# Kernel optimization log

Measured on AMD Instinct MI355X. Metric: run time of the kernel, lower is better.

## Reference

```python
import jax, jax.numpy as jnp
import numpy as np

NUM_HEADS = 8
NEG_INF = -2**32 + 1  # matches the TF code's masking constant


def setup_inputs() -> dict:
    key = jax.random.key(0)
    ks = jax.random.split(key, 12)
    B, L, D_IN, D_MODEL = 2, 2048, 256, 256
    s = 1.0 / np.sqrt(D_IN)
    return {
        "queries": jax.random.normal(ks[0], (B, L, D_IN), jnp.float32),
        "keys": jax.random.normal(ks[1], (B, L, D_IN), jnp.float32),
        "values": jax.random.normal(ks[2], (B, L, D_IN), jnp.float32),
        "key_mask": jax.random.randint(ks[3], (B, L, 1), 0, 2, jnp.int32),
        "Wq": jax.random.normal(ks[4], (D_IN, D_MODEL), jnp.float32) * s,
        "bq": jnp.zeros((D_MODEL,), jnp.float32),
        "Wk": jax.random.normal(ks[5], (D_IN, D_MODEL), jnp.float32) * s,
        "bk": jnp.zeros((D_MODEL,), jnp.float32),
        "Wv": jax.random.normal(ks[6], (D_IN, D_MODEL), jnp.float32) * s,
        "bv": jnp.zeros((D_MODEL,), jnp.float32),
        "Wo": jax.random.normal(ks[7], (D_MODEL, D_IN), jnp.float32) * s,
        "bo": jnp.zeros((D_IN,), jnp.float32),
    }


def reference(queries, keys, values, key_mask, Wq, bq, Wk, bk, Wv, bv, Wo, bo):
    B, Lq, _ = queries.shape
    Lk = keys.shape[1]
    h = NUM_HEADS
    d_model = Wq.shape[1]
    depth = d_model // h

    Q = queries @ Wq + bq  # [B, Lq, d_model]
    K = keys @ Wk + bk     # [B, Lk, d_model]
    V = values @ Wv + bv   # [B, Lk, d_model]

    # split heads: contiguous chunks of size depth along feature dim
    Qh = Q.reshape(B, Lq, h, depth)
    Kh = K.reshape(B, Lk, h, depth)
    Vh = V.reshape(B, Lk, h, depth)

    scores = jnp.einsum("bqhd,bkhd->bhqk", Qh, Kh) / jnp.sqrt(
        jnp.asarray(depth, jnp.float32)
    )  # [B, h, Lq, Lk]

    # key_mask: [B, Lk, 1] -> broadcast over heads and query positions
    mask = (key_mask[:, None, :, 0] != 0)[:, :, None, :]  # [B, 1, 1, Lk]
    scores = jnp.where(mask, scores, jnp.asarray(NEG_INF, scores.dtype))

    attn = jax.nn.softmax(scores, axis=-1)  # dropout is identity at inference
    out = jnp.einsum("bhqk,bkhd->bqhd", attn, Vh).reshape(B, Lq, d_model)
    return out @ Wo + bo  # [B, Lq, input_dim]
```

## Files before the change

kernel.cpp:

```cpp
#include <hip/hip_runtime.h>

#define Bn 2
#define Ln 2048
#define DIN 256
#define Hn 8
#define DEPTH 32
#define SCALE 0.17677669529663687f
#define NEGC (-4294967296.0f)
#define NG  (Ln / 16)
#define WLS 264

typedef _Float16 f16;
typedef _Float16 h8 __attribute__((ext_vector_type(8)));
typedef _Float16 h4 __attribute__((ext_vector_type(4)));
typedef float f4 __attribute__((ext_vector_type(4)));


__global__ __launch_bounds__(256) void proj_gemm(
    const float* __restrict__ Xq, const float* __restrict__ Xk, const float* __restrict__ Xv,
    const float* __restrict__ Wq, const float* __restrict__ Wk, const float* __restrict__ Wv,
    const float* __restrict__ bq, const float* __restrict__ bk, const float* __restrict__ bv,
    f16* __restrict__ Qz, f16* __restrict__ Kz, f16* __restrict__ Vz)
{
    const int p = blockIdx.z;
    const float* X = p == 0 ? Xq : p == 1 ? Xk : Xv;
    const float* W = p == 0 ? Wq : p == 1 ? Wk : Wv;
    const float* bias = p == 0 ? bq : p == 1 ? bk : bv;

    const int t = threadIdx.x, w = t >> 6, lane = t & 63;
    const int l15 = lane & 15, quad = lane >> 4;
    const int n0 = blockIdx.y * 64;
    const int m0 = blockIdx.x * 64 + w * 16;

    const float* A0 = X + (size_t)(m0 + l15) * DIN;
    const float* Wp = W + n0 + l15;

    f4 acc[4] = {{0.f,0.f,0.f,0.f},{0.f,0.f,0.f,0.f},
                 {0.f,0.f,0.f,0.f},{0.f,0.f,0.f,0.f}};
    #pragma unroll
    for (int kk = 0; kk < 8; ++kk) {
        const int k0 = kk * 32;
        float4 xa = *(const float4*)(A0 + k0 + quad * 8);
        float4 xb = *(const float4*)(A0 + k0 + quad * 8 + 4);
        h8 af = { (f16)xa.x, (f16)xa.y, (f16)xa.z, (f16)xa.w,
                  (f16)xb.x, (f16)xb.y, (f16)xb.z, (f16)xb.w };
        h8 bf[4];
        #pragma unroll
        for (int tt = 0; tt < 4; ++tt)
            #pragma unroll
            for (int j = 0; j < 8; ++j)
                bf[tt][j] = (f16)Wp[(size_t)(k0 + quad * 8 + j) * DIN + tt * 16];
        #pragma unroll
        for (int tt = 0; tt < 4; ++tt)
            acc[tt] = __builtin_amdgcn_mfma_f32_16x16x32_f16(af, bf[tt], acc[tt], 0, 0, 0);
    }
    #pragma unroll
    for (int tt = 0; tt < 4; ++tt) {
        const int c = n0 + tt * 16 + l15;
        const float bb = bias[c];
        const int h = c >> 5, dd = c & 31;
        #pragma unroll
        for (int r = 0; r < 4; ++r) {
            const int row = m0 + quad * 4 + r;
            const int b = row >> 11, l = row & (Ln - 1);
            const float v = acc[tt][r] + bb;
            const size_t hbg = (size_t)(b * Hn + h) * NG + (l >> 4);
            if (p == 0)
                Qz[(hbg * 64 + (dd >> 3) * 16 + (l & 15)) * 8 + (dd & 7)] =
                    (f16)(v * SCALE);
            else if (p == 1)
                Kz[(hbg * 64 + (dd >> 3) * 16 + (l & 15)) * 8 + (dd & 7)] = (f16)v;
            else
                Vz[((hbg * 2 + (dd >> 4)) * 64 + ((l & 15) >> 2) * 16 + (dd & 15)) * 4
                   + (l & 3)] = (f16)v;
        }
    }
}

__global__ __launch_bounds__(512) void flash_mfma(
    const f16* __restrict__ Qz, const f16* __restrict__ Kz,
    const f16* __restrict__ Vz, const int* __restrict__ mask,
    f16* __restrict__ Oz)
{
    __shared__ float Os[8][32][34];
    __shared__ float lS[8][32];
    const int t = threadIdx.x, w = t >> 6, lane = t & 63;
    const int l15 = lane & 15, quad = lane >> 4;
    const int bid = blockIdx.x;
    const int swz = (bid & 7) * 128 + (bid >> 3);
    const int hb = swz >> 6, qc = swz & 63;
    const int q0 = qc * 32;
    const int b = hb >> 3, h = hb & 7;
    const f16* Qh = Qz + (size_t)hb * NG * 512;
    const f16* Kh = Kz + (size_t)hb * NG * 512;
    const f16* Vh = Vz + (size_t)hb * NG * 512;
    const int* mrow = mask + b * Ln;
    const int k_base = w * (Ln / 8);

    h8 qf[2];
    #pragma unroll
    for (int qg = 0; qg < 2; ++qg)
        qf[qg] = *(const h8*)(Qh + ((size_t)(qc * 2 + qg) * 64 + lane) * 8);

    f4 o[2][2];
    #pragma unroll
    for (int i = 0; i < 2; ++i)
        #pragma unroll
        for (int j = 0; j < 2; ++j) o[i][j] = (f4){0.f, 0.f, 0.f, 0.f};
    float l_run[2] = {0.f, 0.f};

    for (int kt = 0; kt < Ln / 8 / 64; ++kt) {
        const int k0 = k_base + kt * 64;
        #pragma unroll
        for (int tt = 0; tt < 4; ++tt) {
            const int g = (k0 >> 4) + tt;
            h8 kf = *(const h8*)(Kh + ((size_t)g * 64 + lane) * 8);
            const int4 mk = *(const int4*)(mrow + g * 16 + quad * 4);
            f4 bias4 = { mk.x ? 0.f : NEGC, mk.y ? 0.f : NEGC,
                         mk.z ? 0.f : NEGC, mk.w ? 0.f : NEGC };
            h4 va0 = *(const h4*)(Vh + ((size_t)(g * 2)     * 64 + lane) * 4);
            h4 va1 = *(const h4*)(Vh + ((size_t)(g * 2 + 1) * 64 + lane) * 4);
            f4 s[2];
            #pragma unroll
            for (int qg = 0; qg < 2; ++qg)
                s[qg] = __builtin_amdgcn_mfma_f32_16x16x32_f16(kf, qf[qg], bias4, 0, 0, 0);
            #pragma unroll
            for (int qg = 0; qg < 2; ++qg) {
                h4 pf;
                #pragma unroll
                for (int r = 0; r < 4; ++r) {
                    const float pv = __expf(s[qg][r]);
                    l_run[qg] += pv;
                    pf[r] = (f16)pv;
                }
                o[0][qg] = __builtin_amdgcn_mfma_f32_16x16x16f16(va0, pf, o[0][qg], 0, 0, 0);
                o[1][qg] = __builtin_amdgcn_mfma_f32_16x16x16f16(va1, pf, o[1][qg], 0, 0, 0);
            }
        }
    }
    #pragma unroll
    for (int qg = 0; qg < 2; ++qg) {
        l_run[qg] += __shfl_xor(l_run[qg], 16, 64);
        l_run[qg] += __shfl_xor(l_run[qg], 32, 64);
        if (quad == 0) lS[w][qg * 16 + l15] = l_run[qg];
        #pragma unroll
        for (int dg = 0; dg < 2; ++dg)
            #pragma unroll
            for (int r = 0; r < 4; ++r)
                Os[w][dg * 16 + quad * 4 + r][qg * 16 + l15] = o[dg][qg][r];
    }
    __syncthreads();

    if (t < 128) {
        const int cq = t & 31, dv = t >> 5;
        float ls = 0.f;
        #pragma unroll
        for (int i = 0; i < 8; ++i) ls += lS[i][cq];
        const float inv = 1.0f / ls;
        h8 pack;
        #pragma unroll
        for (int i = 0; i < 8; ++i) {
            const int dd = dv * 8 + i;
            float ov = 0.f;
            #pragma unroll
            for (int s = 0; s < 8; ++s) ov += Os[s][dd][cq];
            pack[i] = (f16)(ov * inv);
        }
        const int gm = b * NG + ((q0 + cq) >> 4);
        *(h8*)(Oz + (((size_t)gm * 8 + h) * 64 + dv * 16 + (cq & 15)) * 8) = pack;
    }
}

__global__ __launch_bounds__(256) void out_gemm(
    const f16* __restrict__ Oz, const float* __restrict__ Wo,
    const float* __restrict__ bo, float* __restrict__ out)
{
    const int t = threadIdx.x, w = t >> 6, lane = t & 63;
    const int l15 = lane & 15, quad = lane >> 4;
    const int g = blockIdx.x >> 1, nh = blockIdx.x & 1;

    h8 af[8];
    #pragma unroll
    for (int h = 0; h < 8; ++h)
        af[h] = *(const h8*)(Oz + (((size_t)g * 8 + h) * 64 + lane) * 8);

    const float* Wop = Wo + nh * 128 + w * 32 + l15;
    f4 acc[2] = {{0.f,0.f,0.f,0.f},{0.f,0.f,0.f,0.f}};
    #pragma unroll
    for (int h = 0; h < 8; ++h) {
        h8 bf[2];
        #pragma unroll
        for (int tt = 0; tt < 2; ++tt)
            #pragma unroll
            for (int j = 0; j < 8; ++j)
                bf[tt][j] = (f16)Wop[(size_t)(h * 32 + quad * 8 + j) * DIN + tt * 16];
        #pragma unroll
        for (int tt = 0; tt < 2; ++tt)
            acc[tt] = __builtin_amdgcn_mfma_f32_16x16x32_f16(af[h], bf[tt], acc[tt], 0, 0, 0);
    }
    #pragma unroll
    for (int tt = 0; tt < 2; ++tt) {
        const int c = nh * 128 + w * 32 + tt * 16 + l15;
        const float bb = bo[c];
        #pragma unroll
        for (int r = 0; r < 4; ++r)
            out[(size_t)(g * 16 + quad * 4 + r) * DIN + c] = acc[tt][r] + bb;
    }
}

__global__ __launch_bounds__(256) void fb_projKV(
    const float* __restrict__ Xk, const float* __restrict__ Xv,
    const float* __restrict__ Wk, const float* __restrict__ Wv,
    const float* __restrict__ bk, const float* __restrict__ bv,
    f16* S, int b)
{
    __shared__ f16 Wl[64 * WLS];
    const int p = blockIdx.z;
    const float* X = (p ? Xv : Xk) + (size_t)b * Ln * DIN;
    const float* W = p ? Wv : Wk;
    const float* bias = p ? bv : bk;

    const int t = threadIdx.x, w = t >> 6, lane = t & 63;
    const int l15 = lane & 15, quad = lane >> 4;
    const int n0 = blockIdx.y * 64;

    {
        const int nl = t & 63, kb = t >> 6;
        for (int kk = 0; kk < 64; ++kk) {
            const int k = kk * 4 + kb;
            Wl[nl * WLS + k] = (f16)W[(size_t)k * DIN + n0 + nl];
        }
    }
    __syncthreads();

    const int m0w = blockIdx.x * 128 + w * 32;
    const float* A0 = X + (size_t)(m0w + l15) * DIN;
    const float* A1 = X + (size_t)(m0w + 16 + l15) * DIN;

    f4 acc[2][4];
    #pragma unroll
    for (int mi = 0; mi < 2; ++mi)
        #pragma unroll
        for (int tt = 0; tt < 4; ++tt) acc[mi][tt] = (f4){0.f, 0.f, 0.f, 0.f};

    for (int k0 = 0; k0 < DIN; k0 += 32) {
        float4 xa0 = *(const float4*)(A0 + k0 + quad * 8);
        float4 xb0 = *(const float4*)(A0 + k0 + quad * 8 + 4);
        float4 xa1 = *(const float4*)(A1 + k0 + quad * 8);
        float4 xb1 = *(const float4*)(A1 + k0 + quad * 8 + 4);
        h8 af0 = { (f16)xa0.x, (f16)xa0.y, (f16)xa0.z, (f16)xa0.w,
                   (f16)xb0.x, (f16)xb0.y, (f16)xb0.z, (f16)xb0.w };
        h8 af1 = { (f16)xa1.x, (f16)xa1.y, (f16)xa1.z, (f16)xa1.w,
                   (f16)xb1.x, (f16)xb1.y, (f16)xb1.z, (f16)xb1.w };
        #pragma unroll
        for (int tt = 0; tt < 4; ++tt) {
            h8 bf = *(const h8*)(Wl + (tt * 16 + l15) * WLS + k0 + quad * 8);
            acc[0][tt] = __builtin_amdgcn_mfma_f32_16x16x32_f16(af0, bf, acc[0][tt], 0, 0, 0);
            acc[1][tt] = __builtin_amdgcn_mfma_f32_16x16x32_f16(af1, bf, acc[1][tt], 0, 0, 0);
        }
    }
    #pragma unroll
    for (int mi = 0; mi < 2; ++mi)
        #pragma unroll
        for (int tt = 0; tt < 4; ++tt) {
            const int c = n0 + tt * 16 + l15;
            const float bb = bias[c];
            const int h = c >> 5, dd = c & 31;
            #pragma unroll
            for (int r = 0; r < 4; ++r) {
                const int l = m0w + mi * 16 + quad * 4 + r;
                const float v = acc[mi][tt][r] + bb;
                const unsigned hg = (unsigned)h * 128 + (l >> 4);
                unsigned j;
                if (!p)
                    j = (hg * 64 + (unsigned)(dd >> 3) * 16 + (l & 15)) * 8 + (dd & 7);
                else
                    j = 524288u + ((hg * 2 + (dd >> 4)) * 64
                        + (unsigned)((l & 15) >> 2) * 16 + (dd & 15)) * 4 + (l & 3);
                S[(((size_t)(j >> 12)) << 13) + 4096u + (j & 4095u)] = (f16)v;
            }
        }
}

__global__ __launch_bounds__(512) void fb_flashQ(
    const float* __restrict__ Xq, const float* __restrict__ Wq,
    const float* __restrict__ bq, const int* __restrict__ mask,
    float* outbuf, int b)
{
    __shared__ union {
        struct { f16 Wlq[32 * WLS]; f16 Qs[2048]; } a;
        struct { float Os[8][32][68]; float lS[8][64]; } c;
    } sm;
    f16* S = (f16*)outbuf;
    const int t = threadIdx.x, w = t >> 6, lane = t & 63;
    const int l15 = lane & 15, quad = lane >> 4;
    const int h = blockIdx.x, q0 = blockIdx.y * 64;

    {
        const int nl = t & 31, kb = t >> 5;
        for (int kk = 0; kk < 16; ++kk) {
            const int k = kk * 16 + kb;
            sm.a.Wlq[nl * WLS + k] = (f16)Wq[(size_t)k * DIN + h * 32 + nl];
        }
    }
    __syncthreads();

    if (w < 4) {
        const float* A0 = Xq + (size_t)(b * Ln + q0 + w * 16 + l15) * DIN;
        f4 a2[2] = { {0.f,0.f,0.f,0.f}, {0.f,0.f,0.f,0.f} };
        #pragma unroll
        for (int kk = 0; kk < 8; ++kk) {
            const int k0 = kk * 32;
            float4 xa = *(const float4*)(A0 + k0 + quad * 8);
            float4 xb = *(const float4*)(A0 + k0 + quad * 8 + 4);
            h8 af = { (f16)xa.x, (f16)xa.y, (f16)xa.z, (f16)xa.w,
                      (f16)xb.x, (f16)xb.y, (f16)xb.z, (f16)xb.w };
            #pragma unroll
            for (int tt = 0; tt < 2; ++tt) {
                h8 bf = *(const h8*)(sm.a.Wlq + (tt * 16 + l15) * WLS + k0 + quad * 8);
                a2[tt] = __builtin_amdgcn_mfma_f32_16x16x32_f16(af, bf, a2[tt], 0, 0, 0);
            }
        }
        #pragma unroll
        for (int tt = 0; tt < 2; ++tt) {
            const int c = tt * 16 + l15;
            const float bb = bq[h * 32 + c];
            #pragma unroll
            for (int r = 0; r < 4; ++r) {
                const int lc = quad * 4 + r;
                sm.a.Qs[((size_t)w * 64 + (c >> 3) * 16 + lc) * 8 + (c & 7)] =
                    (f16)((a2[tt][r] + bb) * SCALE);
            }
        }
    }
    __syncthreads();
    h8 qf[4];
    #pragma unroll
    for (int qg = 0; qg < 4; ++qg)
        qf[qg] = *(const h8*)(sm.a.Qs + ((size_t)qg * 64 + lane) * 8);
    __syncthreads();

    const int* mrow = mask + b * Ln;
    f4 o[2][4];
    #pragma unroll
    for (int i = 0; i < 2; ++i)
        #pragma unroll
        for (int j = 0; j < 4; ++j) o[i][j] = (f4){0.f, 0.f, 0.f, 0.f};
    float l_run[4] = {0.f, 0.f, 0.f, 0.f};
    const int k_base = w * (Ln / 8);

    for (int kt = 0; kt < Ln / 8 / 64; ++kt) {
        const int k0 = k_base + kt * 64;
        #pragma unroll
        for (int tt = 0; tt < 4; ++tt) {
            const int g = (k0 >> 4) + tt;
            const size_t kaddr = ((size_t)(h * 16 + (g >> 3)) << 13) + 4096u
                               + (size_t)((g & 7) * 512 + lane * 8);
            h8 kf = *(const h8*)(S + kaddr);
            const int4 mk = *(const int4*)(mrow + g * 16 + quad * 4);
            f4 bias4 = { mk.x ? 0.f : NEGC, mk.y ? 0.f : NEGC,
                         mk.z ? 0.f : NEGC, mk.w ? 0.f : NEGC };
            const size_t vaddr = ((size_t)(128 + h * 16 + (g >> 3)) << 13) + 4096u
                               + (size_t)((g & 7) * 512 + lane * 4);
            h4 va0 = *(const h4*)(S + vaddr);
            h4 va1 = *(const h4*)(S + vaddr + 256);
            f4 s_[4];
            #pragma unroll
            for (int qg = 0; qg < 4; ++qg)
                s_[qg] = __builtin_amdgcn_mfma_f32_16x16x32_f16(kf, qf[qg], bias4, 0, 0, 0);
            #pragma unroll
            for (int qg = 0; qg < 4; ++qg) {
                h4 pf;
                #pragma unroll
                for (int r = 0; r < 4; ++r) {
                    const float pv = __expf(s_[qg][r]);
                    l_run[qg] += pv;
                    pf[r] = (f16)pv;
                }
                o[0][qg] = __builtin_amdgcn_mfma_f32_16x16x16f16(va0, pf, o[0][qg], 0, 0, 0);
                o[1][qg] = __builtin_amdgcn_mfma_f32_16x16x16f16(va1, pf, o[1][qg], 0, 0, 0);
            }
        }
    }
    #pragma unroll
    for (int qg = 0; qg < 4; ++qg) {
        l_run[qg] += __shfl_xor(l_run[qg], 16, 64);
        l_run[qg] += __shfl_xor(l_run[qg], 32, 64);
        if (quad == 0) sm.c.lS[w][qg * 16 + l15] = l_run[qg];
        #pragma unroll
        for (int dg = 0; dg < 2; ++dg)
            #pragma unroll
            for (int r = 0; r < 4; ++r)
                sm.c.Os[w][dg * 16 + quad * 4 + r][qg * 16 + l15] = o[dg][qg][r];
    }
    __syncthreads();

    if (t < 256) {
        const int cq = t & 63, dv = t >> 6;
        float ls = 0.f;
        #pragma unroll
        for (int i = 0; i < 8; ++i) ls += sm.c.lS[i][cq];
        const float inv = 1.0f / ls;
        h8 pack;
        #pragma unroll
        for (int i = 0; i < 8; ++i) {
            const int dd = dv * 8 + i;
            float ov = 0.f;
            #pragma unroll
            for (int s = 0; s < 8; ++s) ov += sm.c.Os[s][dd][cq];
            pack[i] = (f16)(ov * inv);
        }
        const int gm = b * 128 + ((q0 + cq) >> 4);
        *(h8*)(S + (size_t)gm * 8192
               + (size_t)(h * 64 + dv * 16 + (cq & 15)) * 8) = pack;
    }
}

__global__ __launch_bounds__(256) void fb_outproj(
    const float* __restrict__ Wo, const float* __restrict__ bo, float* outbuf)
{
    f16* S = (f16*)outbuf;
    const int t = threadIdx.x, w = t >> 6, lane = t & 63;
    const int l15 = lane & 15, quad = lane >> 4;
    const int g = blockIdx.x;

    h8 af[8];
    #pragma unroll
    for (int h = 0; h < 8; ++h)
        af[h] = *(const h8*)(S + (size_t)g * 8192 + (size_t)(h * 64 + lane) * 8);
    __syncthreads();

    const float* Wop = Wo + w * 64 + l15;
    f4 acc[4] = {{0.f,0.f,0.f,0.f},{0.f,0.f,0.f,0.f},
                 {0.f,0.f,0.f,0.f},{0.f,0.f,0.f,0.f}};
    #pragma unroll
    for (int h = 0; h < 8; ++h) {
        h8 bf[4];
        #pragma unroll
        for (int tt = 0; tt < 4; ++tt)
            #pragma unroll
            for (int j = 0; j < 8; ++j)
                bf[tt][j] = (f16)Wop[(size_t)(h * 32 + quad * 8 + j) * DIN + tt * 16];
        #pragma unroll
        for (int tt = 0; tt < 4; ++tt)
            acc[tt] = __builtin_amdgcn_mfma_f32_16x16x32_f16(af[h], bf[tt], acc[tt], 0, 0, 0);
    }
    #pragma unroll
    for (int tt = 0; tt < 4; ++tt) {
        const int c = w * 64 + tt * 16 + l15;
        const float bb = bo[c];
        #pragma unroll
        for (int r = 0; r < 4; ++r)
            outbuf[(size_t)(g * 16 + quad * 4 + r) * DIN + c] = acc[tt][r] + bb;
    }
}

extern "C" void kernel_launch(void* const* d_in, const int* in_sizes, int n_in,
                              void* d_out, int out_size, void* d_ws, size_t ws_size,
                              hipStream_t stream) {
    (void)in_sizes; (void)n_in; (void)out_size;
    const float* Xq = (const float*)d_in[0];
    const float* Xk = (const float*)d_in[1];
    const float* Xv = (const float*)d_in[2];
    const int*  mask = (const int*)d_in[3];
    const float* Wq = (const float*)d_in[4];
    const float* bq = (const float*)d_in[5];
    const float* Wk = (const float*)d_in[6];
    const float* bk = (const float*)d_in[7];
    const float* Wv = (const float*)d_in[8];
    const float* bv = (const float*)d_in[9];
    const float* Wo = (const float*)d_in[10];
    const float* bo = (const float*)d_in[11];
    float* out = (float*)d_out;

    const size_t HB_E = (size_t)Bn * Hn * Ln * DEPTH;
    const size_t need = 4 * HB_E * sizeof(f16);

    if (ws_size >= need) {
        f16* Qz = (f16*)d_ws;
        f16* Kz = Qz + HB_E;
        f16* Vz = Kz + HB_E;
        f16* Oz = Vz + HB_E;
        proj_gemm<<<dim3(Bn * Ln / 64, DIN / 64, 3), 256, 0, stream>>>(
            Xq, Xk, Xv, Wq, Wk, Wv, bq, bk, bv, Qz, Kz, Vz);
        flash_mfma<<<Ln / 32 * Bn * Hn, 512, 0, stream>>>(Qz, Kz, Vz, mask, Oz);
        out_gemm<<<Bn * Ln / 16 * 2, 256, 0, stream>>>(Oz, Wo, bo, out);
    } else {
        f16* S = (f16*)out;
        fb_projKV<<<dim3(16, 4, 2), 256, 0, stream>>>(Xk, Xv, Wk, Wv, bk, bv, S, 0);
        fb_flashQ<<<dim3(8, 32), 512, 0, stream>>>(Xq, Wq, bq, mask, out, 0);
        fb_projKV<<<dim3(16, 4, 2), 256, 0, stream>>>(Xk, Xv, Wk, Wv, bk, bv, S, 1);
        fb_flashQ<<<dim3(8, 32), 512, 0, stream>>>(Xq, Wq, bq, mask, out, 1);
        fb_outproj<<<256, 256, 0, stream>>>(Wo, bo, out);
    }
}
```

Before: 121.2 us.

## Fuse flash attention with output projection in one kernel per query tile

Merges the attention kernel and the output GEMM into a single kernel. Each 1024-thread block now handles all 8 heads for a 32-row query tile, with two waves per head splitting the key range. The normalized per-head outputs are staged in shared memory, and the block then computes the Wo projection directly and writes the final fp32 output. This removes the Oz round trip through global memory and one kernel launch. In exchange the grid shrinks to 128 large blocks, which lowers parallelism, and each block re-reads all of Wo.

```diff
diff --git a/kernel.cpp b/kernel.cpp
--- a/kernel.cpp
+++ b/kernel.cpp
@@ -77,30 +77,33 @@
     }
 }
 
-__global__ __launch_bounds__(512) void flash_mfma(
+__global__ __launch_bounds__(1024) void flash_out(
     const f16* __restrict__ Qz, const f16* __restrict__ Kz,
     const f16* __restrict__ Vz, const int* __restrict__ mask,
-    f16* __restrict__ Oz)
+    const float* __restrict__ Wo, const float* __restrict__ bo,
+    float* __restrict__ out)
 {
-    __shared__ float Os[8][32][34];
-    __shared__ float lS[8][32];
+    __shared__ union {
+        struct { float Os[16][32][34]; float lS[16][32]; } c;
+        f16 Of[32 * 264];
+    } sm;
     const int t = threadIdx.x, w = t >> 6, lane = t & 63;
     const int l15 = lane & 15, quad = lane >> 4;
     const int bid = blockIdx.x;
-    const int swz = (bid & 7) * 128 + (bid >> 3);
-    const int hb = swz >> 6, qc = swz & 63;
-    const int q0 = qc * 32;
-    const int b = hb >> 3, h = hb & 7;
+    const int swz = (bid & 7) * 16 + (bid >> 3);
+    const int b = swz >> 6, qidx = swz & 63;
+    const int q0 = qidx * 32;
+    const int h = w >> 1, half = w & 1;
+    const int hb = b * Hn + h;
     const f16* Qh = Qz + (size_t)hb * NG * 512;
     const f16* Kh = Kz + (size_t)hb * NG * 512;
     const f16* Vh = Vz + (size_t)hb * NG * 512;
     const int* mrow = mask + b * Ln;
-    const int k_base = w * (Ln / 8);
 
     h8 qf[2];
     #pragma unroll
     for (int qg = 0; qg < 2; ++qg)
-        qf[qg] = *(const h8*)(Qh + ((size_t)(qc * 2 + qg) * 64 + lane) * 8);
+        qf[qg] = *(const h8*)(Qh + ((size_t)(qidx * 2 + qg) * 64 + lane) * 8);
 
     f4 o[2][2];
     #pragma unroll
@@ -109,11 +112,10 @@
         for (int j = 0; j < 2; ++j) o[i][j] = (f4){0.f, 0.f, 0.f, 0.f};
     float l_run[2] = {0.f, 0.f};
 
-    for (int kt = 0; kt < Ln / 8 / 64; ++kt) {
-        const int k0 = k_base + kt * 64;
+    for (int kt = 0; kt < 16; ++kt) {
         #pragma unroll
         for (int tt = 0; tt < 4; ++tt) {
-            const int g = (k0 >> 4) + tt;
+            const int g = half * 64 + kt * 4 + tt;
             h8 kf = *(const h8*)(Kh + ((size_t)g * 64 + lane) * 8);
             const int4 mk = *(const int4*)(mrow + g * 16 + quad * 4);
             f4 bias4 = { mk.x ? 0.f : NEGC, mk.y ? 0.f : NEGC,
@@ -142,69 +144,63 @@
     for (int qg = 0; qg < 2; ++qg) {
         l_run[qg] += __shfl_xor(l_run[qg], 16, 64);
         l_run[qg] += __shfl_xor(l_run[qg], 32, 64);
-        if (quad == 0) lS[w][qg * 16 + l15] = l_run[qg];
+        if (quad == 0) sm.c.lS[w][qg * 16 + l15] = l_run[qg];
         #pragma unroll
         for (int dg = 0; dg < 2; ++dg)
             #pragma unroll
             for (int r = 0; r < 4; ++r)
-                Os[w][dg * 16 + quad * 4 + r][qg * 16 + l15] = o[dg][qg][r];
-    }
-    __syncthreads();
-
-    if (t < 128) {
-        const int cq = t & 31, dv = t >> 5;
-        float ls = 0.f;
-        #pragma unroll
-        for (int i = 0; i < 8; ++i) ls += lS[i][cq];
+                sm.c.Os[w][dg * 16 + quad * 4 + r][qg * 16 + l15] = o[dg][qg][r];
+    }
+    __syncthreads();
+
+    const int cq = t & 31, co = t >> 5;
+    const int ch = co >> 2, dd0 = (co & 3) * 8;
+    h8 opack;
+    {
+        const float ls = sm.c.lS[2 * ch][cq] + sm.c.lS[2 * ch + 1][cq];
         const float inv = 1.0f / ls;
-        h8 pack;
         #pragma unroll
         for (int i = 0; i < 8; ++i) {
-            const int dd = dv * 8 + i;
-            float ov = 0.f;
-            #pragma unroll
-            for (int s = 0; s < 8; ++s) ov += Os[s][dd][cq];
-            pack[i] = (f16)(ov * inv);
-        }
-        const int gm = b * NG + ((q0 + cq) >> 4);
-        *(h8*)(Oz + (((size_t)gm * 8 + h) * 64 + dv * 16 + (cq & 15)) * 8) = pack;
-    }
-}
-
-__global__ __launch_bounds__(256) void out_gemm(
-    const f16* __restrict__ Oz, const float* __restrict__ Wo,
-    const float* __restrict__ bo, float* __restrict__ out)
-{
-    const int t = threadIdx.x, w = t >> 6, lane = t & 63;
-    const int l15 = lane & 15, quad = lane >> 4;
-    const int g = blockIdx.x >> 1, nh = blockIdx.x & 1;
-
-    h8 af[8];
-    #pragma unroll
-    for (int h = 0; h < 8; ++h)
-        af[h] = *(const h8*)(Oz + (((size_t)g * 8 + h) * 64 + lane) * 8);
-
-    const float* Wop = Wo + nh * 128 + w * 32 + l15;
-    f4 acc[2] = {{0.f,0.f,0.f,0.f},{0.f,0.f,0.f,0.f}};
-    #pragma unroll
-    for (int h = 0; h < 8; ++h) {
-        h8 bf[2];
-        #pragma unroll
-        for (int tt = 0; tt < 2; ++tt)
-            #pragma unroll
-            for (int j = 0; j < 8; ++j)
-                bf[tt][j] = (f16)Wop[(size_t)(h * 32 + quad * 8 + j) * DIN + tt * 16];
-        #pragma unroll
-        for (int tt = 0; tt < 2; ++tt)
-            acc[tt] = __builtin_amdgcn_mfma_f32_16x16x32_f16(af[h], bf[tt], acc[tt], 0, 0, 0);
-    }
-    #pragma unroll
-    for (int tt = 0; tt < 2; ++tt) {
-        const int c = nh * 128 + w * 32 + tt * 16 + l15;
-        const float bb = bo[c];
-        #pragma unroll
-        for (int r = 0; r < 4; ++r)
-            out[(size_t)(g * 16 + quad * 4 + r) * DIN + c] = acc[tt][r] + bb;
+            const float ov = sm.c.Os[2 * ch][dd0 + i][cq]
+                           + sm.c.Os[2 * ch + 1][dd0 + i][cq];
+            opack[i] = (f16)(ov * inv);
+        }
+    }
+    __syncthreads();
+    *(h8*)(sm.Of + cq * 264 + co * 8) = opack;
+    __syncthreads();
+
+    {
+        const int rt = w >> 3, tp = w & 7;
+        h8 af[8];
+        #pragma unroll
+        for (int kk = 0; kk < 8; ++kk)
+            af[kk] = *(const h8*)(sm.Of + (rt * 16 + l15) * 264 + kk * 32 + quad * 8);
+
+        const float* Wop = Wo + tp * 32 + l15;
+        f4 acc[2] = {{0.f,0.f,0.f,0.f},{0.f,0.f,0.f,0.f}};
+        #pragma unroll
+        for (int kk = 0; kk < 8; ++kk) {
+            h8 bf[2];
+            #pragma unroll
+            for (int i = 0; i < 2; ++i)
+                #pragma unroll
+                for (int j = 0; j < 8; ++j)
+                    bf[i][j] = (f16)Wop[(size_t)(kk * 32 + quad * 8 + j) * DIN + i * 16];
+            #pragma unroll
+            for (int i = 0; i < 2; ++i)
+                acc[i] = __builtin_amdgcn_mfma_f32_16x16x32_f16(af[kk], bf[i], acc[i], 0, 0, 0);
+        }
+        #pragma unroll
+        for (int i = 0; i < 2; ++i) {
+            const int c = tp * 32 + i * 16 + l15;
+            const float bb = bo[c];
+            #pragma unroll
+            for (int r = 0; r < 4; ++r) {
+                const int row = q0 + rt * 16 + quad * 4 + r;
+                out[(size_t)(b * Ln + row) * DIN + c] = acc[i][r] + bb;
+            }
+        }
     }
 }
 
@@ -474,17 +470,16 @@
     float* out = (float*)d_out;
 
     const size_t HB_E = (size_t)Bn * Hn * Ln * DEPTH;
-    const size_t need = 4 * HB_E * sizeof(f16);
+    const size_t need = 3 * HB_E * sizeof(f16);
 
     if (ws_size >= need) {
         f16* Qz = (f16*)d_ws;
         f16* Kz = Qz + HB_E;
         f16* Vz = Kz + HB_E;
-        f16* Oz = Vz + HB_E;
         proj_gemm<<<dim3(Bn * Ln / 64, DIN / 64, 3), 256, 0, stream>>>(
             Xq, Xk, Xv, Wq, Wk, Wv, bq, bk, bv, Qz, Kz, Vz);
-        flash_mfma<<<Ln / 32 * Bn * Hn, 512, 0, stream>>>(Qz, Kz, Vz, mask, Oz);
-        out_gemm<<<Bn * Ln / 16 * 2, 256, 0, stream>>>(Oz, Wo, bo, out);
+        flash_out<<<Bn * Ln / 32, 1024, 0, stream>>>(
+            Qz, Kz, Vz, mask, Wo, bo, out);
     } else {
         f16* S = (f16*)out;
         fb_projKV<<<dim3(16, 4, 2), 256, 0, stream>>>(Xk, Xv, Wk, Wv, bk, bv, S, 0);
```

After: 134.0 us. 10.5% more time.
